# Kernel optimization log

Measured on AMD Instinct MI355X. Metric: run time of the kernel, lower is better.

Reference implementation:

```python
import jax, jax.numpy as jnp
import numpy as np

C = 256      # in_channels
H = 16       # num_heads
K = 7        # tconv kernel size
P1 = 8       # type_1 partition size
P2 = 8       # type_2 partition size
HB = H // 4  # heads per attention branch (= 4)
EPS = 1e-5


def _ln(x, g, b):
    m = x.mean(-1, keepdims=True)
    v = ((x - m) ** 2).mean(-1, keepdims=True)
    return (x - m) / jnp.sqrt(v + EPS) * g + b


def _window_attn(parts, table, heads, P):
    # parts: [B_, P, 3*Cb]; table: [2P-1, heads]
    B_, N, _ = parts.shape
    qkv = parts.reshape(B_, N, 3, heads, -1).transpose(2, 0, 3, 1, 4)  # [3,B_,h,P,d]
    q, k, v = qkv[0], qkv[1], qkv[2]
    scale = heads ** (-0.5)  # NOTE: module scales by num_heads**-0.5 (faithful)
    attn = jnp.einsum('bhnd,bhmd->bhnm', q * scale, k)
    idx = (jnp.arange(P)[:, None] - jnp.arange(P)[None, :]) + P - 1  # [P,P]
    bias = table[idx].transpose(2, 0, 1)  # [h,P,P]
    attn = jax.nn.softmax(attn + bias[None], axis=-1)
    out = jnp.einsum('bhnm,bhmd->bhnd', attn, v)
    return out.transpose(0, 2, 1, 3).reshape(B_, N, -1)


def _type1_part(x, P):  # x: [B,Cc,T] contiguous windows
    B, Cc, T = x.shape
    return x.reshape(B, Cc, T // P, P).transpose(0, 2, 3, 1).reshape(-1, P, Cc)


def _type1_rev(y, B, Cc, T, P):
    return y.reshape(B, T // P, P, Cc).transpose(0, 3, 1, 2).reshape(B, Cc, T)


def _type2_part(x, P):  # strided (dilated) windows
    B, Cc, T = x.shape
    return x.reshape(B, Cc, P, T // P).transpose(0, 3, 2, 1).reshape(-1, P, Cc)


def _type2_rev(y, B, Cc, T, P):
    return y.reshape(B, T // P, P, Cc).transpose(0, 3, 2, 1).reshape(B, Cc, T)


def setup_inputs() -> dict:
    key = jax.random.key(0)
    ks = jax.random.split(key, 16)
    B, T = 16, 8192
    d = {
        'x': jax.random.normal(ks[0], (B, C, T), jnp.float32),
        'g1': jnp.ones((C,), jnp.float32),
        'b1': jnp.zeros((C,), jnp.float32),
        'Wm': jax.random.normal(ks[1], (C, 2 * C), jnp.float32) * 0.02,
        'bm': jnp.zeros((2 * C,), jnp.float32),
        'Wc': jax.random.normal(ks[2], (C // 2, (C // 2) // (H // 2), K), jnp.float32) * 0.05,
        'bc': jnp.zeros((C // 2,), jnp.float32),
        'tab1': jax.random.normal(ks[3], (2 * P1 - 1, HB), jnp.float32) * 0.02,
        'tab2': jax.random.normal(ks[4], (2 * P2 - 1, HB), jnp.float32) * 0.02,
        'Wp': jax.random.normal(ks[5], (C, C), jnp.float32) * 0.02,
        'bp': jnp.zeros((C,), jnp.float32),
        'g2': jnp.ones((C,), jnp.float32),
        'b2': jnp.zeros((C,), jnp.float32),
        'W1': jax.random.normal(ks[6], (C, 4 * C), jnp.float32) * 0.02,
        'bf1': jnp.zeros((4 * C,), jnp.float32),
        'W2': jax.random.normal(ks[7], (4 * C, C), jnp.float32) * 0.02,
        'bf2': jnp.zeros((C,), jnp.float32),
    }
    return d


def _forward(x, g1, b1, Wm, bm, Wc, bc, tab1, tab2, Wp, bp, g2, b2, W1, bf1, W2, bf2):
    B, Cin, T = x.shape
    xt = x.transpose(0, 2, 1)  # [B,T,C]
    skip = xt
    f = (_ln(xt, g1, b1) @ Wm + bm).transpose(0, 2, 1)  # [B,2C,T]
    f_conv, f_attn = f[:, :Cin // 2], f[:, Cin // 2:]
    # grouped temporal conv, padding SAME
    y0 = jax.lax.conv_general_dilated(
        f_conv, Wc, window_strides=(1,), padding=[((K - 1) // 2, (K - 1) // 2)],
        feature_group_count=H // 2, dimension_numbers=('NCH', 'OIH', 'NCH')) + bc[None, :, None]
    Cb3 = 3 * Cin // 4
    fa1, fa2 = f_attn[:, :Cb3], f_attn[:, Cb3:]
    y1 = _type1_rev(_window_attn(_type1_part(fa1, P1), tab1, HB, P1), B, Cin // 4, T, P1)
    y2 = _type2_rev(_window_attn(_type2_part(fa2, P2), tab2, HB, P2), B, Cin // 4, T, P2)
    out = jnp.concatenate([y0, y1, y2], axis=1).transpose(0, 2, 1) @ Wp + bp
    out = skip + out
    h = _ln(out, g2, b2)
    h = jax.nn.gelu(h @ W1 + bf1, approximate=False) @ W2 + bf2
    out = out + h
    return out.transpose(0, 2, 1)  # [B,C,T]


def reference(x, g1, b1, Wm, bm, Wc, bc, tab1, tab2, Wp, bp, g2, b2, W1, bf1, W2, bf2):
    return _forward(x, g1, b1, Wm, bm, Wc, bc, tab1, tab2, Wp, bp, g2, b2, W1, bf1, W2, bf2)
```

## Files before the change

kernel.cpp:

```cpp
#include <hip/hip_runtime.h>
#include <hip/hip_bf16.h>

#define DI __device__ __forceinline__

typedef unsigned short u16;
typedef __attribute__((ext_vector_type(4))) float f32x4;
typedef __attribute__((ext_vector_type(8))) short short8;
typedef __attribute__((ext_vector_type(4))) short short4v;

constexpr int Bb = 16, Tt = 8192;
constexpr int M_TOT = Bb * Tt;

static DI u16 f2bf(float f) {
    union { float f; unsigned u; } v; v.f = f;
    unsigned r = v.u + 0x7fffu + ((v.u >> 16) & 1u);
    return (u16)(r >> 16);
}
static DI float bf2f(u16 u) {
    union { unsigned u; float f; } v; v.u = ((unsigned)u) << 16;
    return v.f;
}
static DI float bf2f_s(short s) { return bf2f((u16)s); }

static DI void lds_load16(const void* g, void* l) {
    __builtin_amdgcn_global_load_lds(
        (const __attribute__((address_space(1))) void*)g,
        (__attribute__((address_space(3))) void*)l, 16, 0, 0);
}

static DI float gelu_fast(float x) {
    float x2 = x * x;
    float z2 = x * (2.30220723f + 0.10294515f * x2);
    float e;
    asm("v_exp_f32 %0, %1" : "=v"(e) : "v"(z2));
    float r = __builtin_amdgcn_rcpf(1.f + e);
    return x - x * r;
}

__global__ void prep_weights(const float* __restrict__ Wm, const float* __restrict__ Wp,
                             const float* __restrict__ W1, const float* __restrict__ W2,
                             const float* __restrict__ Wc,
                             const float* __restrict__ g1, const float* __restrict__ b1,
                             const float* __restrict__ g2, const float* __restrict__ b2,
                             const float* __restrict__ bm, const float* __restrict__ bf1,
                             u16* __restrict__ WmT, u16* __restrict__ WpT,
                             u16* __restrict__ W1T, u16* __restrict__ W2T,
                             u16* __restrict__ WtC,
                             float* __restrict__ bmF, float* __restrict__ b1F,
                             float* __restrict__ colsum) {
    int i = blockIdx.x * blockDim.x + threadIdx.x;
    int stride = gridDim.x * blockDim.x;
    for (int j = i; j < 512 * 256; j += stride) {
        int n = j >> 8, k = j & 255;
        WmT[j] = f2bf(Wm[k * 512 + n] * g1[k]);
    }
    for (int j = i; j < 256 * 256; j += stride) {
        int n = j >> 8, k = j & 255;
        WpT[j] = f2bf(Wp[k * 256 + n]);
    }
    for (int j = i; j < 1024 * 256; j += stride) {
        int n = j >> 8, k = j & 255;
        W1T[j] = f2bf(W1[k * 1024 + n] * g2[k]);
    }
    for (int j = i; j < 256 * 1024; j += stride) {
        int n = j >> 10, k = j & 1023;
        W2T[j] = f2bf(W2[k * 256 + n]);
    }
    for (int j = i; j < 128 * 128; j += stride) {
        int co = j >> 7, kp = j & 127;
        int tap = kp >> 4, ci = kp & 15;
        float v = (tap < 7) ? Wc[(co * 16 + ci) * 7 + tap] : 0.f;
        WtC[j] = f2bf(v);
    }
    for (int n = i; n < 512; n += stride) {
        float s = bm[n], cs = 0.f;
        for (int k = 0; k < 256; ++k) {
            s += b1[k] * Wm[k * 512 + n];
            cs += g1[k] * Wm[k * 512 + n];
        }
        bmF[n] = s;
        colsum[n] = cs;
    }
    for (int n = i; n < 1024; n += stride) {
        float s = bf1[n];
        for (int k = 0; k < 256; ++k) s += b2[k] * W1[k * 1024 + n];
        b1F[n] = s;
    }
}

__global__ __launch_bounds__(256) void ln1_kernel(const float* __restrict__ x,
                                                  u16* __restrict__ xt,
                                                  float* __restrict__ mbuf,
                                                  float* __restrict__ rbuf) {
    __shared__ u16 tile[64 * 256];
    __shared__ float ps[64 * 16], pss[64 * 16];
    int bidx = blockIdx.x;
    int b = bidx >> 7;
    int t0 = (bidx & 127) << 6;
    int tid = threadIdx.x, l = tid & 63, w = tid >> 6;
    int lr = l & 15, lg = l >> 4;
    float s[4] = {}, ss[4] = {};
    #pragma unroll 4
    for (int it = 0; it < 16; ++it) {
        int c = it * 16 + w * 4 + lg;
        f32x4 v = *(const f32x4*)&x[((size_t)b * 256 + c) * 8192 + t0 + lr * 4];
        #pragma unroll
        for (int k = 0; k < 4; ++k) {
            s[k] += v[k]; ss[k] += v[k] * v[k];
            int t = lr * 4 + k;
            int c8 = c >> 3;
            int slot = (c8 & 24) | ((c8 ^ t) & 7);
            tile[t * 256 + slot * 8 + (c & 7)] = f2bf(v[k]);
        }
    }
    #pragma unroll
    for (int k = 0; k < 4; ++k) {
        ps[(lr * 4 + k) * 16 + w * 4 + lg] = s[k];
        pss[(lr * 4 + k) * 16 + w * 4 + lg] = ss[k];
    }
    __syncthreads();
    if (tid < 64) {
        float sum = 0.f, sq = 0.f;
        #pragma unroll
        for (int g = 0; g < 16; ++g) { sum += ps[tid * 16 + g]; sq += pss[tid * 16 + g]; }
        float m = sum * (1.f / 256.f);
        mbuf[(size_t)b * 8192 + t0 + tid] = m;
        rbuf[(size_t)b * 8192 + t0 + tid] = rsqrtf(sq * (1.f / 256.f) - m * m + 1e-5f);
    }
    int r = tid >> 2, q = tid & 3;
    size_t rowbase = ((size_t)b * 8192 + t0 + r) * 256;
    #pragma unroll
    for (int u = 0; u < 8; ++u) {
        int c0 = q * 64 + u * 8;
        int c8 = c0 >> 3;
        int slot = (c8 & 24) | ((c8 ^ r) & 7);
        short8 d = *(const short8*)&tile[r * 256 + slot * 8];
        *(short8*)&xt[rowbase + c0] = d;
    }
}

template<int EPI, int N, int K>
__global__ __launch_bounds__(256) void gemm_bt2(const u16* __restrict__ A,
                                                const u16* __restrict__ Bt,
                                                const float* __restrict__ bias,
                                                u16* __restrict__ outb,
                                                const u16* __restrict__ skipx,
                                                const float* __restrict__ mbuf,
                                                const float* __restrict__ rbuf,
                                                const float* __restrict__ colsum) {
    constexpr int NB = N / 128;
    int bid = blockIdx.x;
    int x8 = bid & 7;
    int rest = bid >> 3;
    int ni = rest % NB;
    int mi = (rest / NB) * 8 + x8;
    int m0 = mi * 128, n0 = ni * 128;
    __shared__ u16 As[2][128 * 64];
    __shared__ u16 Bs[2][128 * 64];
    int tid = threadIdx.x, l = tid & 63, w = tid >> 6;
    int mrow = (w >> 1) * 64, ncol = (w & 1) * 64;
    int lr = l & 15, lg = l >> 4;
    f32x4 acc[4][4] = {};
    auto stage = [&](int buf, int k0) {
        #pragma unroll
        for (int p = 0; p < 4; ++p) {
            int cb = p * 256 + w * 64;
            int chunk = cb + l;
            int row = chunk >> 3, k8 = chunk & 7;
            int k8s = k8 ^ (row & 7);
            lds_load16(A  + (size_t)(m0 + row) * K + k0 + k8s * 8, &As[buf][cb * 8]);
            lds_load16(Bt + (size_t)(n0 + row) * K + k0 + k8s * 8, &Bs[buf][cb * 8]);
        }
    };
    stage(0, 0);
    __syncthreads();
    constexpr int NT = K / 64;
    int buf = 0;
    for (int t = 0; t < NT; ++t) {
        if (t + 1 < NT) stage(buf ^ 1, (t + 1) * 64);
        __builtin_amdgcn_s_setprio(1);
        #pragma unroll
        for (int kk = 0; kk < 64; kk += 32) {
            short8 a[4], bfr[4];
            #pragma unroll
            for (int i = 0; i < 4; ++i) {
                int r = mrow + i * 16 + lr;
                a[i] = *(const short8*)&As[buf][r * 64 + ((((kk >> 3) + lg) ^ (r & 7)) << 3)];
            }
            #pragma unroll
            for (int j = 0; j < 4; ++j) {
                int r = ncol + j * 16 + lr;
                bfr[j] = *(const short8*)&Bs[buf][r * 64 + ((((kk >> 3) + lg) ^ (r & 7)) << 3)];
            }
            #pragma unroll
            for (int i = 0; i < 4; ++i)
                #pragma unroll
                for (int j = 0; j < 4; ++j)
                    acc[i][j] = __builtin_amdgcn_mfma_f32_16x16x32_bf16(a[i], bfr[j], acc[i][j], 0, 0, 0);
        }
        __builtin_amdgcn_s_setprio(0);
        __syncthreads();
        buf ^= 1;
    }
    #pragma unroll
    for (int i = 0; i < 4; ++i) {
        int row0 = m0 + mrow + i * 16 + lg * 4;
        f32x4 mv, rv;
        if constexpr (EPI == 0) {
            mv = *(const f32x4*)&mbuf[row0];
            rv = *(const f32x4*)&rbuf[row0];
        }
        #pragma unroll
        for (int j = 0; j < 4; ++j) {
            int col = n0 + ncol + j * 16 + lr;
            float bv = bias[col];
            f32x4 v = acc[i][j];
            if constexpr (EPI == 0) {
                float cs = colsum[col];
                #pragma unroll
                for (int r = 0; r < 4; ++r)
                    outb[(size_t)(row0 + r) * N + col] =
                        f2bf(rv[r] * (v[r] - mv[r] * cs) + bv);
            } else {
                #pragma unroll
                for (int r = 0; r < 4; ++r)
                    outb[(size_t)(row0 + r) * N + col] =
                        f2bf(v[r] + bv + bf2f(skipx[(size_t)(row0 + r) * 256 + col]));
            }
        }
    }
}

__global__ __launch_bounds__(1024, 1) void ffn_fused7(const u16* __restrict__ outb,
                                                      const u16* __restrict__ W1g,
                                                      const float* __restrict__ b1F,
                                                      const u16* __restrict__ W2T,
                                                      const float* __restrict__ bf2v,
                                                      float* __restrict__ out) {
    __shared__ u16 W1c[2][64 * 256];
    __shared__ u16 W2c[2][256 * 64];
    __shared__ u16 hbuf[128 * 64];
    int bid = blockIdx.x;
    int m0 = bid * 128;
    int tid = threadIdx.x, l = tid & 63, w = tid >> 6;
    int lr = l & 15, lg = l >> 4;
    int wm1 = w >> 1, wn1 = w & 1;
    int wm2 = w >> 2, wn2 = w & 3;

    short8 a_reg[8];
    {
        size_t base = (size_t)(m0 + wm1 * 16 + lr) * 256 + lg * 8;
        float s = 0.f, ss = 0.f;
        #pragma unroll
        for (int ks = 0; ks < 8; ++ks) {
            short8 rv = *(const short8*)&outb[base + ks * 32];
            a_reg[ks] = rv;
            #pragma unroll
            for (int e = 0; e < 8; ++e) { float v = bf2f_s(rv[e]); s += v; ss += v * v; }
        }
        s += __shfl_xor(s, 16); ss += __shfl_xor(ss, 16);
        s += __shfl_xor(s, 32); ss += __shfl_xor(ss, 32);
        float m = s * (1.f / 256.f);
        float rs = rsqrtf(ss * (1.f / 256.f) - m * m + 1e-5f);
        #pragma unroll
        for (int ks = 0; ks < 8; ++ks) {
            short8 rv = a_reg[ks], ov;
            #pragma unroll
            for (int e = 0; e < 8; ++e) ov[e] = (short)f2bf((bf2f_s(rv[e]) - m) * rs);
            a_reg[ks] = ov;
        }
    }

    auto stageW1 = [&](int buf, int c) {
        #pragma unroll
        for (int p = 0; p < 2; ++p) {
            int cb = p * 1024 + w * 64;
            int chunk = cb + l;
            int row = chunk >> 5, sl = chunk & 31;
            int sl2 = (sl & 24) | ((sl ^ row) & 7);
            lds_load16(W1g + (size_t)(c * 64 + row) * 256 + sl2 * 8, &W1c[buf][cb * 8]);
        }
    };
    auto stageW2 = [&](int buf, int c) {
        #pragma unroll
        for (int p = 0; p < 2; ++p) {
            int cb = p * 1024 + w * 64;
            int chunk = cb + l;
            int row = chunk >> 3, sl = chunk & 7;
            int sl2 = sl ^ (row & 7);
            lds_load16(W2T + (size_t)row * 1024 + c * 64 + sl2 * 8, &W2c[buf][cb * 8]);
        }
    };
    stageW1(0, 0); stageW2(0, 0);
    f32x4 acc2[2][4] = {};
    __syncthreads();

    for (int c = 0; c < 16; ++c) {
        int buf = c & 1;
        f32x4 acc1[2] = {};
        __builtin_amdgcn_s_setprio(1);
        #pragma unroll
        for (int ks = 0; ks < 8; ++ks) {
            short8 wf[2];
            #pragma unroll
            for (int nt = 0; nt < 2; ++nt) {
                int n = wn1 * 32 + nt * 16 + lr;
                int sl = ks * 4 + lg;
                int sl2 = (sl & 24) | ((sl ^ n) & 7);
                wf[nt] = *(const short8*)&W1c[buf][n * 256 + sl2 * 8];
            }
            #pragma unroll
            for (int nt = 0; nt < 2; ++nt)
                acc1[nt] = __builtin_amdgcn_mfma_f32_16x16x32_bf16(
                    wf[nt], a_reg[ks], acc1[nt], 0, 0, 0);
        }
        __builtin_amdgcn_s_setprio(0);
        if (c < 15) { stageW1(buf ^ 1, c + 1); stageW2(buf ^ 1, c + 1); }
        #pragma unroll
        for (int nt = 0; nt < 2; ++nt) {
            int colb = wn1 * 32 + nt * 16 + lg * 4;
            int row = wm1 * 16 + lr;
            f32x4 bv4 = *(const f32x4*)&b1F[c * 64 + colb];
            float g0 = gelu_fast(acc1[nt][0] + bv4[0]);
            float g1v = gelu_fast(acc1[nt][1] + bv4[1]);
            float g2v = gelu_fast(acc1[nt][2] + bv4[2]);
            float g3v = gelu_fast(acc1[nt][3] + bv4[3]);
            uint2 dd;
            asm("v_cvt_pk_bf16_f32 %0, %1, %2" : "=v"(dd.x) : "v"(g0), "v"(g1v));
            asm("v_cvt_pk_bf16_f32 %0, %1, %2" : "=v"(dd.y) : "v"(g2v), "v"(g3v));
            int sl2 = (colb >> 3) ^ (row & 7);
            *(uint2*)&hbuf[row * 64 + sl2 * 8 + (colb & 7)] = dd;
        }
        asm volatile("s_waitcnt lgkmcnt(0)" ::: "memory");
        __builtin_amdgcn_s_barrier();
        __builtin_amdgcn_sched_barrier(0);
        __builtin_amdgcn_s_setprio(1);
        #pragma unroll
        for (int ks = 0; ks < 2; ++ks) {
            short8 hf[2], w2f[4];
            #pragma unroll
            for (int mt = 0; mt < 2; ++mt) {
                int row = wm2 * 32 + mt * 16 + lr;
                int sl2 = (ks * 4 + lg) ^ (row & 7);
                hf[mt] = *(const short8*)&hbuf[row * 64 + sl2 * 8];
            }
            #pragma unroll
            for (int nt = 0; nt < 4; ++nt) {
                int n = wn2 * 64 + nt * 16 + lr;
                int sl2 = (ks * 4 + lg) ^ (n & 7);
                w2f[nt] = *(const short8*)&W2c[buf][n * 64 + sl2 * 8];
            }
            #pragma unroll
            for (int mt = 0; mt < 2; ++mt)
                #pragma unroll
                for (int nt = 0; nt < 4; ++nt)
                    acc2[mt][nt] = __builtin_amdgcn_mfma_f32_16x16x32_bf16(
                        hf[mt], w2f[nt], acc2[mt][nt], 0, 0, 0);
        }
        __builtin_amdgcn_s_setprio(0);
        __syncthreads();
    }
    int bb_ = m0 >> 13;
    int tb = m0 & 8191;
    #pragma unroll
    for (int mt = 0; mt < 2; ++mt) {
        int row0 = wm2 * 32 + mt * 16 + lg * 4;
        #pragma unroll
        for (int nt = 0; nt < 4; ++nt) {
            int col = wn2 * 64 + nt * 16 + lr;
            float bv = bf2v[col];
            f32x4 o;
            #pragma unroll
            for (int r = 0; r < 4; ++r)
                o[r] = acc2[mt][nt][r] + bv + bf2f(outb[(size_t)(m0 + row0 + r) * 256 + col]);
            *(f32x4*)&out[((size_t)bb_ * 256 + col) * 8192 + tb + row0] = o;
        }
    }
}

__global__ __launch_bounds__(256) void mixer_kernel(const u16* __restrict__ f,
                                                    const u16* __restrict__ WtC,
                                                    const float* __restrict__ bc,
                                                    const float* __restrict__ tab1,
                                                    const float* __restrict__ tab2,
                                                    u16* __restrict__ att) {
    __shared__ u16 smem[25600];
    __shared__ float stab[60];
    int bid = blockIdx.x;
    int path = bid % 3;
    int inner = bid / 3;
    int b = inner >> 7;
    int tid = threadIdx.x, l = tid & 63, w = tid >> 6;

    if (path == 0) {
        u16* fs = smem;
        u16* wt = smem + 9216;
        int t0 = (inner & 127) << 6;
        #pragma unroll
        for (int k = 0; k < 8; ++k) {
            int c = tid + k * 256;
            int row = c >> 4, sl = c & 15;
            int c8s = (sl & 8) | ((sl ^ row) & 7);
            lds_load16(WtC + row * 128 + c8s * 8, &wt[(w * 64 + (tid & 63)) * 8 + k * 256 * 8]);
        }
        for (int c = tid; c < 72 * 16; c += 256) {
            int rrow = c >> 4, c8 = c & 15;
            int t = t0 - 3 + rrow;
            uint4 v = {0u, 0u, 0u, 0u};
            if (t >= 0 && t < 8192)
                v = *(const uint4*)&f[((size_t)b * 8192 + t) * 512 + c8 * 8];
            int slot = (c8 & 8) | ((c8 ^ rrow) & 7);
            *(uint4*)&fs[rrow * 128 + slot * 8] = v;
        }
        __syncthreads();
        int wr = w >> 1, wc = w & 1;
        int lr = l & 15, lg = l >> 4;
        f32x4 acc[2][4] = {};
        #pragma unroll
        for (int kk = 0; kk < 4; ++kk) {
            int kp = kk * 32 + lg * 8;
            int tap = kp >> 4, ci = kp & 15;
            #pragma unroll
            for (int i = 0; i < 2; ++i) {
                int trow = wr * 32 + i * 16 + lr;
                #pragma unroll
                for (int g = 0; g < 4; ++g) {
                    int ra = trow + tap;
                    int ea = (wc * 4 + g) * 2 + (ci >> 3);
                    short8 a = *(const short8*)&fs[ra * 128 + (((ea & 8) | ((ea ^ ra) & 7)) << 3)];
                    int nb = (wc * 4 + g) * 16 + lr;
                    int eb = kp >> 3;
                    short8 bfr = *(const short8*)&wt[nb * 128 + (((eb & 8) | ((eb ^ nb) & 7)) << 3)];
                    acc[i][g] = __builtin_amdgcn_mfma_f32_16x16x32_bf16(a, bfr, acc[i][g], 0, 0, 0);
                }
            }
        }
        #pragma unroll
        for (int i = 0; i < 2; ++i) {
            int trow = wr * 32 + i * 16 + lg * 4;
            #pragma unroll
            for (int g = 0; g < 4; ++g) {
                int co = (wc * 4 + g) * 16 + lr;
                float bv = bc[co];
                #pragma unroll
                for (int r = 0; r < 4; ++r) {
                    int t = t0 + trow + r;
                    att[((size_t)b * 8192 + t) * 256 + co] = f2bf(acc[i][g][r] + bv);
                }
            }
        }
    } else {
        u16* qkv = smem;
        const int QBASE = (path == 1) ? 128 : 320;
        const int OBASE = (path == 1) ? 128 : 192;
        const float* tab = (path == 1) ? tab1 : tab2;
        int j0 = (inner & 127) << 3;
        if (tid < 60) stab[tid] = tab[tid];
        for (int c = tid; c < 64 * 24; c += 256) {
            int ridx = c / 24, off = (c % 24) << 3;
            int wl = ridx >> 3, n = ridx & 7;
            int t = (path == 1) ? ((j0 + wl) * 8 + n) : (n * 1024 + j0 + wl);
            *(uint4*)&qkv[ridx * 200 + off] = *(const uint4*)&f[((size_t)b * 8192 + t) * 512 + QBASE + off];
        }
        __syncthreads();
        int wl = tid >> 5, h = (tid >> 3) & 3, n = tid & 7;
        const u16* qr = &qkv[(wl * 8 + n) * 200 + h * 16];
        float q[16];
        {
            short8 q0 = *(const short8*)qr, q1 = *(const short8*)(qr + 8);
            #pragma unroll
            for (int d = 0; d < 8; ++d) { q[d] = bf2f_s(q0[d]); q[d + 8] = bf2f_s(q1[d]); }
        }
        float s[8];
        #pragma unroll
        for (int m = 0; m < 8; ++m) {
            const u16* kr = &qkv[(wl * 8 + m) * 200 + 64 + h * 16];
            short8 k0 = *(const short8*)kr, k1 = *(const short8*)(kr + 8);
            float a = 0.f;
            #pragma unroll
            for (int d = 0; d < 8; ++d) a += q[d] * bf2f_s(k0[d]) + q[d + 8] * bf2f_s(k1[d]);
            s[m] = 0.5f * a + stab[(n - m + 7) * 4 + h];
        }
        float mx = s[0];
        #pragma unroll
        for (int m = 1; m < 8; ++m) mx = fmaxf(mx, s[m]);
        float sum = 0.f;
        #pragma unroll
        for (int m = 0; m < 8; ++m) { s[m] = __expf(s[m] - mx); sum += s[m]; }
        float rinv = 1.f / sum;
        float o[16] = {};
        #pragma unroll
        for (int m = 0; m < 8; ++m) {
            float p = s[m] * rinv;
            const u16* vr = &qkv[(wl * 8 + m) * 200 + 128 + h * 16];
            short8 v0 = *(const short8*)vr, v1 = *(const short8*)(vr + 8);
            #pragma unroll
            for (int d = 0; d < 8; ++d) { o[d] += p * bf2f_s(v0[d]); o[d + 8] += p * bf2f_s(v1[d]); }
        }
        int t = (path == 1) ? ((j0 + wl) * 8 + n) : (n * 1024 + j0 + wl);
        short8 o0, o1;
        #pragma unroll
        for (int d = 0; d < 8; ++d) { o0[d] = (short)f2bf(o[d]); o1[d] = (short)f2bf(o[d + 8]); }
        u16* op = &att[((size_t)b * 8192 + t) * 256 + OBASE + h * 16];
        *(short8*)op = o0; *(short8*)(op + 8) = o1;
    }
}

extern "C" void kernel_launch(void* const* d_in, const int* in_sizes, int n_in,
                              void* d_out, int out_size, void* d_ws, size_t ws_size,
                              hipStream_t stream) {
    const float* x    = (const float*)d_in[0];
    const float* g1   = (const float*)d_in[1];
    const float* b1   = (const float*)d_in[2];
    const float* Wm   = (const float*)d_in[3];
    const float* bm   = (const float*)d_in[4];
    const float* Wc   = (const float*)d_in[5];
    const float* bc   = (const float*)d_in[6];
    const float* tab1 = (const float*)d_in[7];
    const float* tab2 = (const float*)d_in[8];
    const float* Wp   = (const float*)d_in[9];
    const float* bp   = (const float*)d_in[10];
    const float* g2   = (const float*)d_in[11];
    const float* b2   = (const float*)d_in[12];
    const float* W1   = (const float*)d_in[13];
    const float* bf1  = (const float*)d_in[14];
    const float* W2   = (const float*)d_in[15];
    const float* bf2  = (const float*)d_in[16];
    float* out = (float*)d_out;

    char* ws = (char*)d_ws;
    u16* f    = (u16*)(ws);
    u16* att  = (u16*)(ws + 134217728);
    u16* outb = (u16*)(ws + 201326592);
    u16* xt   = (u16*)(ws + 335544320);
    char* wb = ws + 402653184;
    u16* WmT    = (u16*)wb;
    u16* WpT    = (u16*)(wb + 262144);
    u16* W1T    = (u16*)(wb + 393216);
    u16* W2T    = (u16*)(wb + 917504);
    u16* WtC    = (u16*)(wb + 1441792);
    float* bmF  = (float*)(wb + 1474560);
    float* b1F  = (float*)(wb + 1476608);
    float* cs1  = (float*)(wb + 1480704);
    float* mbuf = (float*)(wb + 1482752);
    float* rbuf = (float*)(wb + 2007040);

    prep_weights<<<512, 256, 0, stream>>>(Wm, Wp, W1, W2, Wc, g1, b1, g2, b2, bm, bf1,
                                          WmT, WpT, W1T, W2T, WtC, bmF, b1F, cs1);
    ln1_kernel<<<Bb * (Tt / 64), 256, 0, stream>>>(x, xt, mbuf, rbuf);
    gemm_bt2<0, 512, 256><<<(M_TOT / 128) * 4, 256, 0, stream>>>(xt, WmT, bmF, f, nullptr,
                                                                 mbuf, rbuf, cs1);
    mixer_kernel<<<3 * Bb * 128, 256, 0, stream>>>(f, WtC, bc, tab1, tab2, att);
    gemm_bt2<1, 256, 256><<<(M_TOT / 128) * 2, 256, 0, stream>>>(att, WpT, bp, outb, xt,
                                                                 nullptr, nullptr, nullptr);
    ffn_fused7<<<M_TOT / 128, 1024, 0, stream>>>(outb, W1T, b1F, W2T, bf2, out);
}
```

Baseline: 462.5 us.

## Fuse Wp projection GEMM with residual into the FFN kernel

Removes the separate Wp projection GEMM launch and computes it at the start of the FFN kernel for each 128-row tile. Shared memory is reused between the projection and FFN stages. The residual-added result is still written to the outb global buffer, then read back by the same block after a barrier, where it is likely to hit in cache. This drops one kernel launch and its tail, but the projection now runs at the FFN kernel's one-block-per-CU occupancy, so latency hiding may be weaker.

```diff
diff --git a/kernel.cpp b/kernel.cpp
--- a/kernel.cpp
+++ b/kernel.cpp
@@ -139,12 +139,11 @@
     }
 }
 
-template<int EPI, int N, int K>
+template<int N, int K>
 __global__ __launch_bounds__(256) void gemm_bt2(const u16* __restrict__ A,
                                                 const u16* __restrict__ Bt,
                                                 const float* __restrict__ bias,
                                                 u16* __restrict__ outb,
-                                                const u16* __restrict__ skipx,
                                                 const float* __restrict__ mbuf,
                                                 const float* __restrict__ rbuf,
                                                 const float* __restrict__ colsum) {
@@ -205,45 +204,108 @@
     #pragma unroll
     for (int i = 0; i < 4; ++i) {
         int row0 = m0 + mrow + i * 16 + lg * 4;
-        f32x4 mv, rv;
-        if constexpr (EPI == 0) {
-            mv = *(const f32x4*)&mbuf[row0];
-            rv = *(const f32x4*)&rbuf[row0];
-        }
+        f32x4 mv = *(const f32x4*)&mbuf[row0];
+        f32x4 rv = *(const f32x4*)&rbuf[row0];
         #pragma unroll
         for (int j = 0; j < 4; ++j) {
             int col = n0 + ncol + j * 16 + lr;
             float bv = bias[col];
+            float cs = colsum[col];
             f32x4 v = acc[i][j];
-            if constexpr (EPI == 0) {
-                float cs = colsum[col];
-                #pragma unroll
-                for (int r = 0; r < 4; ++r)
-                    outb[(size_t)(row0 + r) * N + col] =
-                        f2bf(rv[r] * (v[r] - mv[r] * cs) + bv);
-            } else {
-                #pragma unroll
-                for (int r = 0; r < 4; ++r)
-                    outb[(size_t)(row0 + r) * N + col] =
-                        f2bf(v[r] + bv + bf2f(skipx[(size_t)(row0 + r) * 256 + col]));
-            }
-        }
-    }
-}
-
-__global__ __launch_bounds__(1024, 1) void ffn_fused7(const u16* __restrict__ outb,
-                                                      const u16* __restrict__ W1g,
-                                                      const float* __restrict__ b1F,
-                                                      const u16* __restrict__ W2T,
-                                                      const float* __restrict__ bf2v,
-                                                      float* __restrict__ out) {
-    __shared__ u16 W1c[2][64 * 256];
-    __shared__ u16 W2c[2][256 * 64];
-    __shared__ u16 hbuf[128 * 64];
+            #pragma unroll
+            for (int r = 0; r < 4; ++r)
+                outb[(size_t)(row0 + r) * N + col] =
+                    f2bf(rv[r] * (v[r] - mv[r] * cs) + bv);
+        }
+    }
+}
+
+__global__ __launch_bounds__(1024, 1) void wp_ffn(const u16* __restrict__ att,
+                                                  const u16* __restrict__ WpT,
+                                                  const float* __restrict__ bp,
+                                                  const u16* __restrict__ xt,
+                                                  const u16* __restrict__ W1g,
+                                                  const float* __restrict__ b1F,
+                                                  const u16* __restrict__ W2T,
+                                                  const float* __restrict__ bf2v,
+                                                  u16* __restrict__ outb,
+                                                  float* __restrict__ out) {
+    __shared__ u16 smem[73728];
     int bid = blockIdx.x;
     int m0 = bid * 128;
     int tid = threadIdx.x, l = tid & 63, w = tid >> 6;
     int lr = l & 15, lg = l >> 4;
+
+    #define ASP(buf) (&smem[(buf) * 8192])
+    #define BSP(buf) (&smem[16384 + (buf) * 16384])
+    #define W1C(buf) (&smem[(buf) * 16384])
+    #define W2C(buf) (&smem[32768 + (buf) * 16384])
+    #define HBUF     (&smem[65536])
+
+    {
+        int wmP = w >> 2, wnP = w & 3;
+        f32x4 acc[2][4] = {};
+        auto stageP = [&](int buf, int k0) {
+            {
+                int chunk = tid;
+                int row = chunk >> 3, k8 = chunk & 7;
+                int k8s = k8 ^ (row & 7);
+                lds_load16(att + (size_t)(m0 + row) * 256 + k0 + k8s * 8, ASP(buf) + chunk * 8);
+            }
+            #pragma unroll
+            for (int p = 0; p < 2; ++p) {
+                int chunk = p * 1024 + tid;
+                int row = chunk >> 3, k8 = chunk & 7;
+                int k8s = k8 ^ (row & 7);
+                lds_load16(WpT + (size_t)row * 256 + k0 + k8s * 8, BSP(buf) + chunk * 8);
+            }
+        };
+        stageP(0, 0);
+        __syncthreads();
+        int buf = 0;
+        for (int t = 0; t < 4; ++t) {
+            if (t < 3) stageP(buf ^ 1, (t + 1) * 64);
+            __builtin_amdgcn_s_setprio(1);
+            #pragma unroll
+            for (int kk = 0; kk < 64; kk += 32) {
+                short8 a[2], bfr[4];
+                #pragma unroll
+                for (int i = 0; i < 2; ++i) {
+                    int r = wmP * 32 + i * 16 + lr;
+                    a[i] = *(const short8*)(ASP(buf) + r * 64 + ((((kk >> 3) + lg) ^ (r & 7)) << 3));
+                }
+                #pragma unroll
+                for (int j = 0; j < 4; ++j) {
+                    int n = wnP * 64 + j * 16 + lr;
+                    bfr[j] = *(const short8*)(BSP(buf) + n * 64 + ((((kk >> 3) + lg) ^ (n & 7)) << 3));
+                }
+                #pragma unroll
+                for (int i = 0; i < 2; ++i)
+                    #pragma unroll
+                    for (int j = 0; j < 4; ++j)
+                        acc[i][j] = __builtin_amdgcn_mfma_f32_16x16x32_bf16(a[i], bfr[j], acc[i][j], 0, 0, 0);
+            }
+            __builtin_amdgcn_s_setprio(0);
+            __syncthreads();
+            buf ^= 1;
+        }
+        #pragma unroll
+        for (int i = 0; i < 2; ++i) {
+            int row0 = m0 + wmP * 32 + i * 16 + lg * 4;
+            #pragma unroll
+            for (int j = 0; j < 4; ++j) {
+                int col = wnP * 64 + j * 16 + lr;
+                float bv = bp[col];
+                f32x4 v = acc[i][j];
+                #pragma unroll
+                for (int r = 0; r < 4; ++r)
+                    outb[(size_t)(row0 + r) * 256 + col] =
+                        f2bf(v[r] + bv + bf2f(xt[(size_t)(row0 + r) * 256 + col]));
+            }
+        }
+    }
+    __syncthreads();
+
     int wm1 = w >> 1, wn1 = w & 1;
     int wm2 = w >> 2, wn2 = w & 3;
 
@@ -278,7 +340,7 @@
             int chunk = cb + l;
             int row = chunk >> 5, sl = chunk & 31;
             int sl2 = (sl & 24) | ((sl ^ row) & 7);
-            lds_load16(W1g + (size_t)(c * 64 + row) * 256 + sl2 * 8, &W1c[buf][cb * 8]);
+            lds_load16(W1g + (size_t)(c * 64 + row) * 256 + sl2 * 8, W1C(buf) + cb * 8);
         }
     };
     auto stageW2 = [&](int buf, int c) {
@@ -288,7 +350,7 @@
             int chunk = cb + l;
             int row = chunk >> 3, sl = chunk & 7;
             int sl2 = sl ^ (row & 7);
-            lds_load16(W2T + (size_t)row * 1024 + c * 64 + sl2 * 8, &W2c[buf][cb * 8]);
+            lds_load16(W2T + (size_t)row * 1024 + c * 64 + sl2 * 8, W2C(buf) + cb * 8);
         }
     };
     stageW1(0, 0); stageW2(0, 0);
@@ -307,7 +369,7 @@
                 int n = wn1 * 32 + nt * 16 + lr;
                 int sl = ks * 4 + lg;
                 int sl2 = (sl & 24) | ((sl ^ n) & 7);
-                wf[nt] = *(const short8*)&W1c[buf][n * 256 + sl2 * 8];
+                wf[nt] = *(const short8*)(W1C(buf) + n * 256 + sl2 * 8);
             }
             #pragma unroll
             for (int nt = 0; nt < 2; ++nt)
@@ -329,7 +391,7 @@
             asm("v_cvt_pk_bf16_f32 %0, %1, %2" : "=v"(dd.x) : "v"(g0), "v"(g1v));
             asm("v_cvt_pk_bf16_f32 %0, %1, %2" : "=v"(dd.y) : "v"(g2v), "v"(g3v));
             int sl2 = (colb >> 3) ^ (row & 7);
-            *(uint2*)&hbuf[row * 64 + sl2 * 8 + (colb & 7)] = dd;
+            *(uint2*)(HBUF + row * 64 + sl2 * 8 + (colb & 7)) = dd;
         }
         asm volatile("s_waitcnt lgkmcnt(0)" ::: "memory");
         __builtin_amdgcn_s_barrier();
@@ -342,13 +404,13 @@
             for (int mt = 0; mt < 2; ++mt) {
                 int row = wm2 * 32 + mt * 16 + lr;
                 int sl2 = (ks * 4 + lg) ^ (row & 7);
-                hf[mt] = *(const short8*)&hbuf[row * 64 + sl2 * 8];
+                hf[mt] = *(const short8*)(HBUF + row * 64 + sl2 * 8);
             }
             #pragma unroll
             for (int nt = 0; nt < 4; ++nt) {
                 int n = wn2 * 64 + nt * 16 + lr;
                 int sl2 = (ks * 4 + lg) ^ (n & 7);
-                w2f[nt] = *(const short8*)&W2c[buf][n * 64 + sl2 * 8];
+                w2f[nt] = *(const short8*)(W2C(buf) + n * 64 + sl2 * 8);
             }
             #pragma unroll
             for (int mt = 0; mt < 2; ++mt)
@@ -376,6 +438,11 @@
             *(f32x4*)&out[((size_t)bb_ * 256 + col) * 8192 + tb + row0] = o;
         }
     }
+    #undef ASP
+    #undef BSP
+    #undef W1C
+    #undef W2C
+    #undef HBUF
 }
 
 __global__ __launch_bounds__(256) void mixer_kernel(const u16* __restrict__ f,
@@ -401,7 +468,7 @@
             int c = tid + k * 256;
             int row = c >> 4, sl = c & 15;
             int c8s = (sl & 8) | ((sl ^ row) & 7);
-            lds_load16(WtC + row * 128 + c8s * 8, &wt[(w * 64 + (tid & 63)) * 8 + k * 256 * 8]);
+            lds_load16(WtC + row * 128 + c8s * 8, &wt[c * 8]);
         }
         for (int c = tid; c < 72 * 16; c += 256) {
             int rrow = c >> 4, c8 = c & 15;
@@ -548,10 +615,7 @@
     prep_weights<<<512, 256, 0, stream>>>(Wm, Wp, W1, W2, Wc, g1, b1, g2, b2, bm, bf1,
                                           WmT, WpT, W1T, W2T, WtC, bmF, b1F, cs1);
     ln1_kernel<<<Bb * (Tt / 64), 256, 0, stream>>>(x, xt, mbuf, rbuf);
-    gemm_bt2<0, 512, 256><<<(M_TOT / 128) * 4, 256, 0, stream>>>(xt, WmT, bmF, f, nullptr,
-                                                                 mbuf, rbuf, cs1);
+    gemm_bt2<512, 256><<<(M_TOT / 128) * 4, 256, 0, stream>>>(xt, WmT, bmF, f, mbuf, rbuf, cs1);
     mixer_kernel<<<3 * Bb * 128, 256, 0, stream>>>(f, WtC, bc, tab1, tab2, att);
-    gemm_bt2<1, 256, 256><<<(M_TOT / 128) * 2, 256, 0, stream>>>(att, WpT, bp, outb, xt,
-                                                                 nullptr, nullptr, nullptr);
-    ffn_fused7<<<M_TOT / 128, 1024, 0, stream>>>(outb, W1T, b1F, W2T, bf2, out);
-}
+    wp_ffn<<<M_TOT / 128, 1024, 0, stream>>>(att, WpT, bp, xt, W1T, b1F, W2T, bf2, outb, out);
+}
```

Result: slower. 483.1 us (+4.5%).
